# Kernel optimization log

Measured on AMD Instinct MI355X. Metric: run time of the kernel, lower is better.

The kernel has to match this reference:

```python
import jax, jax.numpy as jnp
import numpy as np

L = 9            # number of levels
T = 2097152      # entries per level (table has L*T rows)
F = 2            # features per entry
DOM_LO, DOM_HI = -1.0, 1.0
DOM_LEN = DOM_HI - DOM_LO
P = 262144       # number of query points


def setup_inputs() -> dict:
    key = jax.random.key(0)
    k1, k2 = jax.random.split(key)
    # points strictly inside the domain (-1, 1)
    x = jax.random.uniform(k1, (P, 3), jnp.float32) * 1.98 + (DOM_LO + 0.01)
    table = jax.random.normal(k2, (L * T, F), jnp.float32)  # nn.Embedding default N(0,1)
    return {"x": x, "table": table}


# 8 voxel-corner offsets, same order as the torch module
_OFFSETS = np.array([[0, 0, 0], [1, 0, 0], [0, 1, 0], [1, 1, 0],
                     [0, 0, 1], [1, 0, 1], [0, 1, 1], [1, 1, 1]], dtype=np.float32)


def reference(x, table):
    vs_f = jnp.float32(2.0) ** jnp.arange(L, dtype=jnp.float32)      # [L] voxel_size per level
    vs_i = (2 ** jnp.arange(L)).astype(jnp.int32)                    # [L] int version

    # points -> per-level grid space: [L, P, 3]
    norm = (x - DOM_LO) / DOM_LEN
    g = norm[None, :, :] * vs_f[:, None, None]
    base = jnp.floor(g)                                              # [L, P, 3]

    offs = jnp.asarray(_OFFSETS)                                     # [8, 3]
    corners = base[:, :, None, :] + offs[None, None, :, :]           # [L, P, 8, 3]
    grid_idx = corners.astype(jnp.int32)

    # corner positions back in world space: [L, P, 8, 3]
    grid_pos = corners / vs_f[:, None, None, None] * DOM_LEN + DOM_LO

    # flat embedding index: gx + gy*vs + gz*vs^2 (no hashing, as in source)
    flat = (grid_idx[..., 0]
            + grid_idx[..., 1] * vs_i[:, None, None]
            + grid_idx[..., 2] * (vs_i[:, None, None] ** 2))          # [L, P, 8] int32
    q = table[flat]                                                   # [L, P, 8, F]

    px, py, pz = x[:, 0], x[:, 1], x[:, 2]                            # each [P], broadcast over L
    x1, x2 = grid_pos[:, :, 0, 0], grid_pos[:, :, 1, 0]
    y1, y2 = grid_pos[:, :, 0, 1], grid_pos[:, :, 2, 1]
    z1, z2 = grid_pos[:, :, 0, 2], grid_pos[:, :, 4, 2]

    wx0 = ((x2 - px) / (x2 - x1))[..., None]                          # [L, P, 1]
    wx1 = ((px - x1) / (x2 - x1))[..., None]
    fx0 = wx0 * q[:, :, 0] + wx1 * q[:, :, 1]
    fx1 = wx0 * q[:, :, 2] + wx1 * q[:, :, 3]
    fx2 = wx0 * q[:, :, 4] + wx1 * q[:, :, 5]
    fx3 = wx0 * q[:, :, 6] + wx1 * q[:, :, 7]

    wy0 = ((y2 - py) / (y2 - y1))[..., None]
    wy1 = ((py - y1) / (y2 - y1))[..., None]
    fy0 = wy0 * fx0 + wy1 * fx1
    fy1 = wy0 * fx2 + wy1 * fx3

    wz0 = ((z2 - pz) / (z2 - z1))[..., None]
    wz1 = ((pz - z1) / (z2 - z1))[..., None]
    fz = wz0 * fy0 + wz1 * fy1                                        # [L, P, F]

    return jnp.transpose(fz, (1, 0, 2)).reshape(x.shape[0], L * F)    # [P, L*F]
```

## Files before the change

kernel.cpp:

```cpp
#include <hip/hip_runtime.h>

#define NLVL  9
#define NPTS  262144
#define NBUCK 4096

#define WS_HIST(ws)   ((unsigned*)(ws))
#define WS_OFFS(ws)   ((unsigned*)((char*)(ws) + 16384))
#define WS_BUCKET(ws) ((unsigned*)((char*)(ws) + 32768))
#define WS_PERM(ws)   ((unsigned*)((char*)(ws) + 32768 + (NPTS * 4)))

__device__ __forceinline__ unsigned part3_4(unsigned v) {
    v &= 0xFu;
    v = (v | (v << 4)) & 0x0C3u;
    v = (v | (v << 2)) & 0x249u;
    return v;
}

__device__ __forceinline__ unsigned bucket_of(float px, float py, float pz) {
    int bx = (int)((px + 1.0f) * 8.0f);
    int by = (int)((py + 1.0f) * 8.0f);
    int bz = (int)((pz + 1.0f) * 8.0f);
    bx = min(max(bx, 0), 15); by = min(max(by, 0), 15); bz = min(max(bz, 0), 15);
    return part3_4((unsigned)bx) | (part3_4((unsigned)by) << 1) | (part3_4((unsigned)bz) << 2);
}

__global__ __launch_bounds__(256) void hist_kernel(
    const float* __restrict__ x, unsigned* __restrict__ hist, unsigned* __restrict__ bucket)
{
    const int p = blockIdx.x * blockDim.x + threadIdx.x;
    if (p >= NPTS) return;
    const unsigned b = bucket_of(x[p * 3 + 0], x[p * 3 + 1], x[p * 3 + 2]);
    bucket[p] = b;
    atomicAdd(&hist[b], 1u);
}

__global__ __launch_bounds__(256) void scan_kernel(
    const unsigned* __restrict__ hist, unsigned* __restrict__ offs)
{
    __shared__ unsigned sums[256];
    const int t = threadIdx.x;
    unsigned local[16];
    unsigned s = 0;
    #pragma unroll
    for (int i = 0; i < 16; ++i) { local[i] = hist[t * 16 + i]; s += local[i]; }
    sums[t] = s;
    __syncthreads();
    for (int d = 1; d < 256; d <<= 1) {
        unsigned add = (t >= d) ? sums[t - d] : 0u;
        __syncthreads();
        sums[t] += add;
        __syncthreads();
    }
    unsigned excl = (t == 0) ? 0u : sums[t - 1];
    #pragma unroll
    for (int i = 0; i < 16; ++i) { offs[t * 16 + i] = excl; excl += local[i]; }
}

__global__ __launch_bounds__(256) void scatter_kernel(
    const unsigned* __restrict__ bucket, unsigned* __restrict__ offs, unsigned* __restrict__ perm)
{
    const int p = blockIdx.x * blockDim.x + threadIdx.x;
    if (p >= NPTS) return;
    const unsigned b = bucket[p];
    const unsigned pos = atomicAdd(&offs[b], 1u);
    perm[pos] = (unsigned)p;
}

__global__ __launch_bounds__(256) void hashgrid_enc_kernel(
    const float* __restrict__ x,
    const float* __restrict__ table,
    const unsigned* __restrict__ perm,
    float* __restrict__ out)
{
    const int tid = blockIdx.x * blockDim.x + threadIdx.x;
    if (tid >= NPTS * NLVL) return;
    const int sp = tid / NLVL;
    const int l  = tid - sp * NLVL;
    const int p  = (int)perm[sp];

    const float px = x[p * 3 + 0];
    const float py = x[p * 3 + 1];
    const float pz = x[p * 3 + 2];

    const int   s  = 1 << l;
    const float vs = (float)s;

    const float gx = (px + 1.0f) * 0.5f * vs;
    const float gy = (py + 1.0f) * 0.5f * vs;
    const float gz = (pz + 1.0f) * 0.5f * vs;

    const float bxf = floorf(gx);
    const float byf = floorf(gy);
    const float bzf = floorf(gz);

    const int ix = (int)bxf;
    const int iy = (int)byf;
    const int iz = (int)bzf;

    const float tx = gx - bxf;
    const float ty = gy - byf;
    const float tz = gz - bzf;
    const float ux = 1.0f - tx;
    const float uy = 1.0f - ty;
    const float uz = 1.0f - tz;

    const int s2   = s * s;
    const int f000 = ix + iy * s + iz * s2;

    const float2* __restrict__ tb = (const float2*)table;

    const float2 q0 = tb[f000];
    const float2 q1 = tb[f000 + 1];
    const float2 q2 = tb[f000 + s];
    const float2 q3 = tb[f000 + s + 1];
    const float2 q4 = tb[f000 + s2];
    const float2 q5 = tb[f000 + s2 + 1];
    const float2 q6 = tb[f000 + s2 + s];
    const float2 q7 = tb[f000 + s2 + s + 1];

    const float fx0a = ux * q0.x + tx * q1.x;
    const float fx0b = ux * q0.y + tx * q1.y;
    const float fx1a = ux * q2.x + tx * q3.x;
    const float fx1b = ux * q2.y + tx * q3.y;
    const float fx2a = ux * q4.x + tx * q5.x;
    const float fx2b = ux * q4.y + tx * q5.y;
    const float fx3a = ux * q6.x + tx * q7.x;
    const float fx3b = ux * q6.y + tx * q7.y;

    const float fy0a = uy * fx0a + ty * fx1a;
    const float fy0b = uy * fx0b + ty * fx1b;
    const float fy1a = uy * fx2a + ty * fx3a;
    const float fy1b = uy * fx2b + ty * fx3b;

    float2 r;
    r.x = uz * fy0a + tz * fy1a;
    r.y = uz * fy0b + tz * fy1b;

    ((float2*)out)[p * NLVL + l] = r;
}

extern "C" void kernel_launch(void* const* d_in, const int* in_sizes, int n_in,
                              void* d_out, int out_size, void* d_ws, size_t ws_size,
                              hipStream_t stream) {
    const float* x     = (const float*)d_in[0];
    const float* table = (const float*)d_in[1];
    float* out = (float*)d_out;

    unsigned* hist   = WS_HIST(d_ws);
    unsigned* offs   = WS_OFFS(d_ws);
    unsigned* bucket = WS_BUCKET(d_ws);
    unsigned* perm   = WS_PERM(d_ws);

    hipMemsetAsync(hist, 0, NBUCK * sizeof(unsigned), stream);

    const int pb = 256;
    hist_kernel<<<(NPTS + pb - 1) / pb, pb, 0, stream>>>(x, hist, bucket);
    scan_kernel<<<1, 256, 0, stream>>>(hist, offs);
    scatter_kernel<<<(NPTS + pb - 1) / pb, pb, 0, stream>>>(bucket, offs, perm);

    const int total = NPTS * NLVL;
    hashgrid_enc_kernel<<<(total + pb - 1) / pb, pb, 0, stream>>>(x, table, perm, out);
}
```

Baseline: 279.5 us.

## Refine Morton buckets, pre-sort point coords, and loop all levels per thread

Raises the spatial sort resolution from a 16^3 to a 32^3 Morton grid, so points handled together are closer in space. The scatter step now also writes the sorted coordinates as float4, which lets the encoder read them contiguously instead of through the permutation. The encoder now handles all nine levels for one point in a single thread and writes the whole output row at once, rather than one thread per (point, level). The trade-offs are fewer threads and more registers per thread for memory-latency hiding, plus a larger histogram and scan.

```diff
diff --git a/kernel.cpp b/kernel.cpp
--- a/kernel.cpp
+++ b/kernel.cpp
@@ -2,26 +2,29 @@
 
 #define NLVL  9
 #define NPTS  262144
-#define NBUCK 4096
+#define NBUCK 32768
 
 #define WS_HIST(ws)   ((unsigned*)(ws))
-#define WS_OFFS(ws)   ((unsigned*)((char*)(ws) + 16384))
-#define WS_BUCKET(ws) ((unsigned*)((char*)(ws) + 32768))
-#define WS_PERM(ws)   ((unsigned*)((char*)(ws) + 32768 + (NPTS * 4)))
+#define WS_OFFS(ws)   ((unsigned*)((char*)(ws) + 131072))
+#define WS_BUCKET(ws) ((unsigned*)((char*)(ws) + 262144))
+#define WS_PERM(ws)   ((unsigned*)((char*)(ws) + 262144 + 1048576))
+#define WS_XS(ws)     ((float4*)  ((char*)(ws) + 262144 + 2097152))
 
-__device__ __forceinline__ unsigned part3_4(unsigned v) {
-    v &= 0xFu;
-    v = (v | (v << 4)) & 0x0C3u;
-    v = (v | (v << 2)) & 0x249u;
+__device__ __forceinline__ unsigned part3(unsigned v) {
+    v &= 0x3FFu;
+    v = (v | (v << 16)) & 0x30000FFu;
+    v = (v | (v << 8))  & 0x300F00Fu;
+    v = (v | (v << 4))  & 0x30C30C3u;
+    v = (v | (v << 2))  & 0x9249249u;
     return v;
 }
 
 __device__ __forceinline__ unsigned bucket_of(float px, float py, float pz) {
-    int bx = (int)((px + 1.0f) * 8.0f);
-    int by = (int)((py + 1.0f) * 8.0f);
-    int bz = (int)((pz + 1.0f) * 8.0f);
-    bx = min(max(bx, 0), 15); by = min(max(by, 0), 15); bz = min(max(bz, 0), 15);
-    return part3_4((unsigned)bx) | (part3_4((unsigned)by) << 1) | (part3_4((unsigned)bz) << 2);
+    int bx = (int)((px + 1.0f) * 16.0f);
+    int by = (int)((py + 1.0f) * 16.0f);
+    int bz = (int)((pz + 1.0f) * 16.0f);
+    bx = min(max(bx, 0), 31); by = min(max(by, 0), 31); bz = min(max(bz, 0), 31);
+    return part3((unsigned)bx) | (part3((unsigned)by) << 1) | (part3((unsigned)bz) << 2);
 }
 
 __global__ __launch_bounds__(256) void hist_kernel(
@@ -39,10 +42,8 @@
 {
     __shared__ unsigned sums[256];
     const int t = threadIdx.x;
-    unsigned local[16];
     unsigned s = 0;
-    #pragma unroll
-    for (int i = 0; i < 16; ++i) { local[i] = hist[t * 16 + i]; s += local[i]; }
+    for (int i = 0; i < NBUCK / 256; ++i) s += hist[t * (NBUCK / 256) + i];
     sums[t] = s;
     __syncthreads();
     for (int d = 1; d < 256; d <<= 1) {
@@ -52,91 +53,107 @@
         __syncthreads();
     }
     unsigned excl = (t == 0) ? 0u : sums[t - 1];
-    #pragma unroll
-    for (int i = 0; i < 16; ++i) { offs[t * 16 + i] = excl; excl += local[i]; }
+    for (int i = 0; i < NBUCK / 256; ++i) {
+        offs[t * (NBUCK / 256) + i] = excl;
+        excl += hist[t * (NBUCK / 256) + i];
+    }
 }
 
 __global__ __launch_bounds__(256) void scatter_kernel(
-    const unsigned* __restrict__ bucket, unsigned* __restrict__ offs, unsigned* __restrict__ perm)
+    const float* __restrict__ x,
+    const unsigned* __restrict__ bucket, unsigned* __restrict__ offs,
+    unsigned* __restrict__ perm, float4* __restrict__ xs)
 {
     const int p = blockIdx.x * blockDim.x + threadIdx.x;
     if (p >= NPTS) return;
     const unsigned b = bucket[p];
     const unsigned pos = atomicAdd(&offs[b], 1u);
     perm[pos] = (unsigned)p;
+    float4 v;
+    v.x = x[p * 3 + 0];
+    v.y = x[p * 3 + 1];
+    v.z = x[p * 3 + 2];
+    v.w = 0.0f;
+    xs[pos] = v;
 }
 
-__global__ __launch_bounds__(256) void hashgrid_enc_kernel(
-    const float* __restrict__ x,
+__global__ __launch_bounds__(256) void enc_kernel(
+    const float4* __restrict__ xs,
+    const unsigned* __restrict__ perm,
     const float* __restrict__ table,
-    const unsigned* __restrict__ perm,
     float* __restrict__ out)
 {
-    const int tid = blockIdx.x * blockDim.x + threadIdx.x;
-    if (tid >= NPTS * NLVL) return;
-    const int sp = tid / NLVL;
-    const int l  = tid - sp * NLVL;
-    const int p  = (int)perm[sp];
+    const int sp = blockIdx.x * blockDim.x + threadIdx.x;
+    if (sp >= NPTS) return;
 
-    const float px = x[p * 3 + 0];
-    const float py = x[p * 3 + 1];
-    const float pz = x[p * 3 + 2];
+    const float4 P = xs[sp];
+    const int    p = (int)perm[sp];
 
-    const int   s  = 1 << l;
-    const float vs = (float)s;
-
-    const float gx = (px + 1.0f) * 0.5f * vs;
-    const float gy = (py + 1.0f) * 0.5f * vs;
-    const float gz = (pz + 1.0f) * 0.5f * vs;
-
-    const float bxf = floorf(gx);
-    const float byf = floorf(gy);
-    const float bzf = floorf(gz);
-
-    const int ix = (int)bxf;
-    const int iy = (int)byf;
-    const int iz = (int)bzf;
-
-    const float tx = gx - bxf;
-    const float ty = gy - byf;
-    const float tz = gz - bzf;
-    const float ux = 1.0f - tx;
-    const float uy = 1.0f - ty;
-    const float uz = 1.0f - tz;
-
-    const int s2   = s * s;
-    const int f000 = ix + iy * s + iz * s2;
+    const float nx = (P.x + 1.0f) * 0.5f;
+    const float ny = (P.y + 1.0f) * 0.5f;
+    const float nz = (P.z + 1.0f) * 0.5f;
 
     const float2* __restrict__ tb = (const float2*)table;
 
-    const float2 q0 = tb[f000];
-    const float2 q1 = tb[f000 + 1];
-    const float2 q2 = tb[f000 + s];
-    const float2 q3 = tb[f000 + s + 1];
-    const float2 q4 = tb[f000 + s2];
-    const float2 q5 = tb[f000 + s2 + 1];
-    const float2 q6 = tb[f000 + s2 + s];
-    const float2 q7 = tb[f000 + s2 + s + 1];
+    float2 res[NLVL];
 
-    const float fx0a = ux * q0.x + tx * q1.x;
-    const float fx0b = ux * q0.y + tx * q1.y;
-    const float fx1a = ux * q2.x + tx * q3.x;
-    const float fx1b = ux * q2.y + tx * q3.y;
-    const float fx2a = ux * q4.x + tx * q5.x;
-    const float fx2b = ux * q4.y + tx * q5.y;
-    const float fx3a = ux * q6.x + tx * q7.x;
-    const float fx3b = ux * q6.y + tx * q7.y;
+    #pragma unroll
+    for (int l = 0; l < NLVL; ++l) {
+        const int   s  = 1 << l;
+        const float vs = (float)s;
 
-    const float fy0a = uy * fx0a + ty * fx1a;
-    const float fy0b = uy * fx0b + ty * fx1b;
-    const float fy1a = uy * fx2a + ty * fx3a;
-    const float fy1b = uy * fx2b + ty * fx3b;
+        const float gx = nx * vs;
+        const float gy = ny * vs;
+        const float gz = nz * vs;
 
-    float2 r;
-    r.x = uz * fy0a + tz * fy1a;
-    r.y = uz * fy0b + tz * fy1b;
+        const float bxf = floorf(gx);
+        const float byf = floorf(gy);
+        const float bzf = floorf(gz);
 
-    ((float2*)out)[p * NLVL + l] = r;
+        const int ix = (int)bxf;
+        const int iy = (int)byf;
+        const int iz = (int)bzf;
+
+        const float tx = gx - bxf;
+        const float ty = gy - byf;
+        const float tz = gz - bzf;
+        const float ux = 1.0f - tx;
+        const float uy = 1.0f - ty;
+        const float uz = 1.0f - tz;
+
+        const int s2   = s * s;
+        const int f000 = ix + iy * s + iz * s2;
+
+        const float2 q0 = tb[f000];
+        const float2 q1 = tb[f000 + 1];
+        const float2 q2 = tb[f000 + s];
+        const float2 q3 = tb[f000 + s + 1];
+        const float2 q4 = tb[f000 + s2];
+        const float2 q5 = tb[f000 + s2 + 1];
+        const float2 q6 = tb[f000 + s2 + s];
+        const float2 q7 = tb[f000 + s2 + s + 1];
+
+        const float fx0a = ux * q0.x + tx * q1.x;
+        const float fx0b = ux * q0.y + tx * q1.y;
+        const float fx1a = ux * q2.x + tx * q3.x;
+        const float fx1b = ux * q2.y + tx * q3.y;
+        const float fx2a = ux * q4.x + tx * q5.x;
+        const float fx2b = ux * q4.y + tx * q5.y;
+        const float fx3a = ux * q6.x + tx * q7.x;
+        const float fx3b = ux * q6.y + tx * q7.y;
+
+        const float fy0a = uy * fx0a + ty * fx1a;
+        const float fy0b = uy * fx0b + ty * fx1b;
+        const float fy1a = uy * fx2a + ty * fx3a;
+        const float fy1b = uy * fx2b + ty * fx3b;
+
+        res[l].x = uz * fy0a + tz * fy1a;
+        res[l].y = uz * fy0b + tz * fy1b;
+    }
+
+    float2* o = (float2*)out + (size_t)p * NLVL;
+    #pragma unroll
+    for (int l = 0; l < NLVL; ++l) o[l] = res[l];
 }
 
 extern "C" void kernel_launch(void* const* d_in, const int* in_sizes, int n_in,
@@ -150,14 +167,13 @@
     unsigned* offs   = WS_OFFS(d_ws);
     unsigned* bucket = WS_BUCKET(d_ws);
     unsigned* perm   = WS_PERM(d_ws);
+    float4*   xs     = WS_XS(d_ws);
 
     hipMemsetAsync(hist, 0, NBUCK * sizeof(unsigned), stream);
 
     const int pb = 256;
     hist_kernel<<<(NPTS + pb - 1) / pb, pb, 0, stream>>>(x, hist, bucket);
     scan_kernel<<<1, 256, 0, stream>>>(hist, offs);
-    scatter_kernel<<<(NPTS + pb - 1) / pb, pb, 0, stream>>>(bucket, offs, perm);
-
-    const int total = NPTS * NLVL;
-    hashgrid_enc_kernel<<<(total + pb - 1) / pb, pb, 0, stream>>>(x, table, perm, out);
+    scatter_kernel<<<(NPTS + pb - 1) / pb, pb, 0, stream>>>(x, bucket, offs, perm, xs);
+    enc_kernel<<<(NPTS + pb - 1) / pb, pb, 0, stream>>>(xs, perm, table, out);
 }
```

After: 275.6 us. Within noise of the previous version (-1.4%).
